# Kernel tuning notes

Hardware: AMD Instinct MI355X
Metric: run time of the kernel (lower is better)

Reference implementation:

```python
import jax, jax.numpy as jnp
import numpy as np

N_NODES = 50000
N_EDGES = 800000
N_FEAT = 128
N_HID = 128
N_CLS = 40
BN_EPS = 1e-5


def setup_inputs() -> dict:
    key = jax.random.key(0)
    ks = jax.random.split(key, 8)
    return {
        "x": jax.random.normal(ks[0], (N_NODES, N_FEAT), dtype=jnp.float32),
        "edge_index": jax.random.randint(ks[1], (2, N_EDGES), 0, N_NODES, dtype=jnp.int64),
        "W1l": jax.random.normal(ks[2], (N_HID, N_FEAT), dtype=jnp.float32) / np.sqrt(N_FEAT),
        "b1": jnp.zeros((N_HID,), dtype=jnp.float32),
        "W1r": jax.random.normal(ks[3], (N_HID, N_FEAT), dtype=jnp.float32) / np.sqrt(N_FEAT),
        "gamma": jnp.ones((N_HID,), dtype=jnp.float32),
        "beta": jnp.zeros((N_HID,), dtype=jnp.float32),
        "run_mean": jax.random.normal(ks[4], (N_HID,), dtype=jnp.float32) * 0.1,
        "run_var": jax.random.uniform(ks[5], (N_HID,), dtype=jnp.float32) + 0.5,
        "W2l": jax.random.normal(ks[6], (N_CLS, N_HID), dtype=jnp.float32) / np.sqrt(N_HID),
        "b2": jnp.zeros((N_CLS,), dtype=jnp.float32),
        "W2r": jax.random.normal(ks[7], (N_CLS, N_HID), dtype=jnp.float32) / np.sqrt(N_HID),
    }


def _sage_conv(h, src, dst, n_nodes, inv_deg, Wl, bl, Wr):
    # mean-aggregate neighbor features at each destination node
    agg = jax.ops.segment_sum(h[src], dst, num_segments=n_nodes)  # [N, D]
    agg = agg * inv_deg[:, None]
    # PyG SAGEConv: lin_l(aggr) (with bias) + lin_r(x) (no bias)
    return agg @ Wl.T + bl + h @ Wr.T


def reference(x, edge_index, W1l, b1, W1r, gamma, beta, run_mean, run_var, W2l, b2, W2r):
    src, dst = edge_index[0], edge_index[1]
    n = x.shape[0]
    deg = jax.ops.segment_sum(jnp.ones_like(src, dtype=x.dtype), dst, num_segments=n)
    inv_deg = 1.0 / jnp.maximum(deg, 1.0)
    h = _sage_conv(x, src, dst, n, inv_deg, W1l, b1, W1r)
    # transition: ReLU -> BatchNorm1d (eval: running stats) -> Dropout (identity in eval)
    h = jnp.maximum(h, 0.0)
    h = (h - run_mean) * (gamma / jnp.sqrt(run_var + BN_EPS)) + beta
    out = _sage_conv(h, src, dst, n, inv_deg, W2l, b2, W2r)
    return out
```

## Files before the change

### kernel.cpp

```cpp
#include <hip/hip_runtime.h>

#define N_NODES 50000
#define N_EDGES 800000
#define N_FEAT 128
#define N_HID 128
#define N_CLS 40
#define BN_EPS 1e-5f

#define CSR_STRIDE 64
#define NXCD 8
#define P_NODES 6250
#define CSR_B 1024
#define CSR_BO 128
#define WPACK_B 84
#define XPACK_B 3125

typedef short bf16x8 __attribute__((ext_vector_type(8)));
typedef float f32x4 __attribute__((ext_vector_type(4)));

__device__ __forceinline__ unsigned bfpack(float a, float b) {
    unsigned ua = __float_as_uint(a), ub = __float_as_uint(b);
    ua = (ua + 0x7FFFu + ((ua >> 16) & 1u)) >> 16;
    ub = (ub + 0x7FFFu + ((ub >> 16) & 1u)) >> 16;
    return ua | (ub << 16);
}
__device__ __forceinline__ unsigned short bfr1(float a) {
    unsigned u = __float_as_uint(a);
    u = (u + 0x7FFFu + ((u >> 16) & 1u)) >> 16;
    return (unsigned short)u;
}
__device__ __forceinline__ float bflo(unsigned u) { return __uint_as_float(u << 16); }
__device__ __forceinline__ float bfhi(unsigned u) { return __uint_as_float(u & 0xFFFF0000u); }

__global__ __launch_bounds__(256) void degprep_kernel(
    const int* __restrict__ src, const int* __restrict__ dst,
    int* __restrict__ deg_i, unsigned short* __restrict__ csr_pad,
    const float* __restrict__ W1l, const float* __restrict__ W1r,
    const float* __restrict__ W2l, const float* __restrict__ W2r,
    const float* __restrict__ x, unsigned* __restrict__ WfA,
    unsigned* __restrict__ WfB, unsigned* __restrict__ x_bf16) {
    int b = blockIdx.x;
    int t = threadIdx.x;
    if (b < CSR_B) {
        const int p = b & (NXCD - 1);
        const int bo = b >> 3;
        const int plo = p * P_NODES;
        const int phi = plo + P_NODES;
        const int4* dst4 = (const int4*)dst;
        const int4* src4 = (const int4*)src;
        for (int base = bo * 1024; base < N_EDGES; base += CSR_BO * 1024) {
            int e = base + t * 4;
            if (e < N_EDGES) {
                int4 d4 = dst4[(e >> 2)];
                int4 s4 = src4[(e >> 2)];
                if (d4.x >= plo && d4.x < phi) {
                    int r = atomicAdd(&deg_i[d4.x], 1);
                    if (r < CSR_STRIDE) csr_pad[d4.x * CSR_STRIDE + r] = (unsigned short)s4.x;
                }
                if (d4.y >= plo && d4.y < phi) {
                    int r = atomicAdd(&deg_i[d4.y], 1);
                    if (r < CSR_STRIDE) csr_pad[d4.y * CSR_STRIDE + r] = (unsigned short)s4.y;
                }
                if (d4.z >= plo && d4.z < phi) {
                    int r = atomicAdd(&deg_i[d4.z], 1);
                    if (r < CSR_STRIDE) csr_pad[d4.z * CSR_STRIDE + r] = (unsigned short)s4.z;
                }
                if (d4.w >= plo && d4.w < phi) {
                    int r = atomicAdd(&deg_i[d4.w], 1);
                    if (r < CSR_STRIDE) csr_pad[d4.w * CSR_STRIDE + r] = (unsigned short)s4.w;
                }
            }
        }
        return;
    }
    int i = (b - CSR_B) * 256 + t;
    if (b < CSR_B + WPACK_B) {
        if (i < 16384) {
            int f = i >> 8, r = i & 255;
            int lane = r >> 2, u = r & 3;
            int phase = f >> 5, kc = (f >> 3) & 3, nt = f & 7;
            int k0 = phase * 128 + kc * 32 + (lane >> 4) * 8 + u * 2;
            int n = nt * 16 + (lane & 15);
            float w0, w1;
            if (k0 < 128) {
                w0 = W1l[n * 128 + k0];
                w1 = W1l[n * 128 + k0 + 1];
            } else {
                w0 = W1r[n * 128 + k0 - 128];
                w1 = W1r[n * 128 + k0 - 127];
            }
            WfA[i] = bfpack(w0, w1);
        } else if (i < 21504) {
            int j = i - 16384;
            int f = j >> 8, r = j & 255;
            int lane = r >> 2, u = r & 3;
            int kc = f / 5, nt = f % 5;
            int k0 = kc * 32 + (lane >> 4) * 8 + u * 2;
            int n = nt * 16 + (lane & 15);
            float w0, w1;
            if (n < 40) {
                w0 = W2l[n * 128 + k0];
                w1 = W2l[n * 128 + k0 + 1];
            } else {
                w0 = W2r[(n - 40) * 128 + k0];
                w1 = W2r[(n - 40) * 128 + k0 + 1];
            }
            WfB[j] = bfpack(w0, w1);
        }
    } else {
        int j = (b - CSR_B - WPACK_B) * 256 + t;
        if (j < 800000) {
            const float4* xf = (const float4*)x;
            float4 a = xf[(size_t)j * 2];
            float4 bq = xf[(size_t)j * 2 + 1];
            uint4 o;
            o.x = bfpack(a.x, a.y);
            o.y = bfpack(a.z, a.w);
            o.z = bfpack(bq.x, bq.y);
            o.w = bfpack(bq.z, bq.w);
            ((uint4*)x_bf16)[j] = o;
        }
    }
}

__global__ __launch_bounds__(256) void gather1_kernel(const unsigned short* __restrict__ csr_pad,
                                                      const int* __restrict__ deg_i,
                                                      const unsigned* __restrict__ x_bf16,
                                                      unsigned* __restrict__ agg1b) {
    int sg = threadIdx.x >> 4;
    int li = threadIdx.x & 15;
    int gid = blockIdx.x * 16 + sg;
    if (gid >= N_NODES) return;
    int n = min(deg_i[gid], CSR_STRIDE);
    int beg = gid * CSR_STRIDE;
    int end = beg + n;
    const uint4* xb = (const uint4*)x_bf16;
    float acc[8];
#pragma unroll
    for (int j = 0; j < 8; ++j) acc[j] = 0.f;

    int e = beg;
    for (; e + 7 < end; e += 8) {
        uint4 tv[8];
#pragma unroll
        for (int q = 0; q < 8; ++q) {
            int s = csr_pad[e + q];
            tv[q] = xb[(size_t)s * 16 + li];
        }
#pragma unroll
        for (int q = 0; q < 8; ++q) {
            acc[0] += bflo(tv[q].x); acc[1] += bfhi(tv[q].x);
            acc[2] += bflo(tv[q].y); acc[3] += bfhi(tv[q].y);
            acc[4] += bflo(tv[q].z); acc[5] += bfhi(tv[q].z);
            acc[6] += bflo(tv[q].w); acc[7] += bfhi(tv[q].w);
        }
    }
    if (e + 3 < end) {
        uint4 tv[4];
#pragma unroll
        for (int q = 0; q < 4; ++q) {
            int s = csr_pad[e + q];
            tv[q] = xb[(size_t)s * 16 + li];
        }
#pragma unroll
        for (int q = 0; q < 4; ++q) {
            acc[0] += bflo(tv[q].x); acc[1] += bfhi(tv[q].x);
            acc[2] += bflo(tv[q].y); acc[3] += bfhi(tv[q].y);
            acc[4] += bflo(tv[q].z); acc[5] += bfhi(tv[q].z);
            acc[6] += bflo(tv[q].w); acc[7] += bfhi(tv[q].w);
        }
        e += 4;
    }
    for (; e < end; ++e) {
        int s = csr_pad[e];
        uint4 t0 = xb[(size_t)s * 16 + li];
        acc[0] += bflo(t0.x); acc[1] += bfhi(t0.x);
        acc[2] += bflo(t0.y); acc[3] += bfhi(t0.y);
        acc[4] += bflo(t0.z); acc[5] += bfhi(t0.z);
        acc[6] += bflo(t0.w); acc[7] += bfhi(t0.w);
    }
    float inv = 1.0f / fmaxf((float)n, 1.0f);
    uint4 o;
    o.x = bfpack(acc[0] * inv, acc[1] * inv);
    o.y = bfpack(acc[2] * inv, acc[3] * inv);
    o.z = bfpack(acc[4] * inv, acc[5] * inv);
    o.w = bfpack(acc[6] * inv, acc[7] * inv);
    ((uint4*)agg1b)[(size_t)gid * 16 + li] = o;
}

__global__ __launch_bounds__(256) void gemm_fused_kernel(
    const unsigned* __restrict__ agg1b, const unsigned* __restrict__ xb,
    const unsigned* __restrict__ WfA, const unsigned* __restrict__ WfB,
    const float* __restrict__ b1,
    const float* __restrict__ gamma, const float* __restrict__ beta,
    const float* __restrict__ rmean, const float* __restrict__ rvar,
    unsigned short* __restrict__ z2s, float* __restrict__ p2) {
    __shared__ unsigned Asu[64 * 68];
    const int t = threadIdx.x;
    const int wid = __builtin_amdgcn_readfirstlane(t >> 6);
    const int lane = t & 63;
    const int li = lane & 15;
    const int quad = lane >> 4;
    const int mbase = blockIdx.x * 64;

    f32x4 dacc[8];
#pragma unroll
    for (int nt = 0; nt < 8; ++nt) dacc[nt] = (f32x4){0.f, 0.f, 0.f, 0.f};

    for (int phase = 0; phase < 2; ++phase) {
        const unsigned* __restrict__ A = phase ? xb : agg1b;
        __syncthreads();
#pragma unroll
        for (int i = 0; i < 4; ++i) {
            int e = i * 256 + t;
            int row = e >> 4, seg = e & 15;
            int rr = mbase + row;
            rr = (rr < N_NODES) ? rr : N_NODES - 1;
            uint4 v = ((const uint4*)A)[(size_t)rr * 16 + seg];
            *(uint4*)&Asu[row * 68 + seg * 4] = v;
        }
        __syncthreads();
        bf16x8 af[4];
#pragma unroll
        for (int kc = 0; kc < 4; ++kc)
            af[kc] = *(const bf16x8*)&Asu[(wid * 16 + li) * 68 + kc * 16 + quad * 4];

        const unsigned* __restrict__ Wp = WfA + phase * 8192;
#pragma unroll
        for (int nt = 0; nt < 8; ++nt) {
#pragma unroll
            for (int kc = 0; kc < 4; ++kc) {
                bf16x8 bfr = *(const bf16x8*)(Wp + (size_t)(kc * 8 + nt) * 256 + lane * 4);
                dacc[nt] = __builtin_amdgcn_mfma_f32_16x16x32_bf16(af[kc], bfr, dacc[nt], 0, 0, 0);
            }
        }
    }

    __syncthreads();
    unsigned short* Hs = (unsigned short*)Asu;
#pragma unroll
    for (int nt = 0; nt < 8; ++nt) {
        int cg = nt * 16 + li;
        float sc = gamma[cg] * rsqrtf(rvar[cg] + BN_EPS);
        float sh = fmaf(-rmean[cg], sc, beta[cg]);
        float bb = b1[cg];
#pragma unroll
        for (int r = 0; r < 4; ++r) {
            int row = wid * 16 + quad * 4 + r;
            float pre = dacc[nt][r] + bb;
            Hs[row * 136 + cg] = bfr1(fmaf(fmaxf(pre, 0.f), sc, sh));
        }
    }
    __syncthreads();

    bf16x8 af2[4];
#pragma unroll
    for (int kc = 0; kc < 4; ++kc)
        af2[kc] = *(const bf16x8*)&Asu[(wid * 16 + li) * 68 + kc * 16 + quad * 4];

    f32x4 d2[5];
#pragma unroll
    for (int nt = 0; nt < 5; ++nt) d2[nt] = (f32x4){0.f, 0.f, 0.f, 0.f};
#pragma unroll
    for (int nt = 0; nt < 5; ++nt) {
#pragma unroll
        for (int kc = 0; kc < 4; ++kc) {
            bf16x8 bfr = *(const bf16x8*)(WfB + (size_t)(kc * 5 + nt) * 256 + lane * 4);
            d2[nt] = __builtin_amdgcn_mfma_f32_16x16x32_bf16(af2[kc], bfr, d2[nt], 0, 0, 0);
        }
    }

#pragma unroll
    for (int nt = 0; nt < 5; ++nt) {
        int cg = nt * 16 + li;
#pragma unroll
        for (int r = 0; r < 4; ++r) {
            int row = mbase + wid * 16 + quad * 4 + r;
            if (row < N_NODES) {
                float vv = d2[nt][r];
                if (cg < 40) z2s[(size_t)row * 40 + cg] = bfr1(vv);
                else p2[(size_t)row * 40 + (cg - 40)] = vv;
            }
        }
    }
}

__global__ __launch_bounds__(256) void gather2_kernel(const unsigned short* __restrict__ csr_pad,
                                                      const int* __restrict__ deg_i,
                                                      const unsigned short* __restrict__ z2s,
                                                      const float* __restrict__ p2,
                                                      const float* __restrict__ b2,
                                                      float* __restrict__ out) {
    int t = threadIdx.x;
    int sub = t / 10;
    int li = t - sub * 10;
    if (sub >= 25) return;
    int gid = blockIdx.x * 25 + sub;
    if (gid >= N_NODES) return;
    int n = min(deg_i[gid], CSR_STRIDE);
    int beg = gid * CSR_STRIDE;
    int end = beg + n;
    const uint2* z2 = (const uint2*)z2s;
    float4 acc = {0.f, 0.f, 0.f, 0.f};
    int e = beg;
    for (; e + 7 < end; e += 8) {
        uint2 tv[8];
#pragma unroll
        for (int q = 0; q < 8; ++q) {
            int s = csr_pad[e + q];
            tv[q] = z2[(size_t)s * 10 + li];
        }
#pragma unroll
        for (int q = 0; q < 8; ++q) {
            acc.x += bflo(tv[q].x); acc.y += bfhi(tv[q].x);
            acc.z += bflo(tv[q].y); acc.w += bfhi(tv[q].y);
        }
    }
    if (e + 3 < end) {
        uint2 tv[4];
#pragma unroll
        for (int q = 0; q < 4; ++q) {
            int s = csr_pad[e + q];
            tv[q] = z2[(size_t)s * 10 + li];
        }
#pragma unroll
        for (int q = 0; q < 4; ++q) {
            acc.x += bflo(tv[q].x); acc.y += bfhi(tv[q].x);
            acc.z += bflo(tv[q].y); acc.w += bfhi(tv[q].y);
        }
        e += 4;
    }
    for (; e < end; ++e) {
        int s = csr_pad[e];
        uint2 t0 = z2[(size_t)s * 10 + li];
        acc.x += bflo(t0.x); acc.y += bfhi(t0.x);
        acc.z += bflo(t0.y); acc.w += bfhi(t0.y);
    }
    float inv = 1.0f / fmaxf((float)n, 1.0f);
    float4 p = ((const float4*)p2)[(size_t)gid * 10 + li];
    float4 bb = ((const float4*)b2)[li];
    float4 r;
    r.x = fmaf(acc.x, inv, p.x + bb.x);
    r.y = fmaf(acc.y, inv, p.y + bb.y);
    r.z = fmaf(acc.z, inv, p.z + bb.z);
    r.w = fmaf(acc.w, inv, p.w + bb.w);
    ((float4*)out)[(size_t)gid * 10 + li] = r;
}

extern "C" void kernel_launch(void* const* d_in, const int* in_sizes, int n_in,
                              void* d_out, int out_size, void* d_ws, size_t ws_size,
                              hipStream_t stream) {
    const float* x     = (const float*)d_in[0];
    const int*   ei    = (const int*)d_in[1];
    const float* W1l   = (const float*)d_in[2];
    const float* b1    = (const float*)d_in[3];
    const float* W1r   = (const float*)d_in[4];
    const float* gamma = (const float*)d_in[5];
    const float* beta  = (const float*)d_in[6];
    const float* rmean = (const float*)d_in[7];
    const float* rvar  = (const float*)d_in[8];
    const float* W2l   = (const float*)d_in[9];
    const float* b2    = (const float*)d_in[10];
    const float* W2r   = (const float*)d_in[11];
    float* out = (float*)d_out;

    int* deg_i              = (int*)d_ws;
    unsigned short* csr_pad = (unsigned short*)(deg_i + 50048);
    unsigned* WfA           = (unsigned*)(deg_i + 50048 + 1600000);
    unsigned* WfB           = WfA + 16384;
    unsigned* x_bf16        = WfB + 5120;
    unsigned* agg1b         = x_bf16 + 3200000;
    unsigned short* z2s     = (unsigned short*)(agg1b + (size_t)50048 * 64);
    float* p2               = (float*)(z2s + (size_t)50048 * 40);

    const int* src = ei;
    const int* dst = ei + N_EDGES;

    hipMemsetAsync(deg_i, 0, (size_t)50048 * sizeof(int), stream);

    degprep_kernel<<<CSR_B + WPACK_B + XPACK_B, 256, 0, stream>>>(
        src, dst, deg_i, csr_pad, W1l, W1r, W2l, W2r, x, WfA, WfB, x_bf16);

    gather1_kernel<<<(N_NODES + 15) / 16, 256, 0, stream>>>(csr_pad, deg_i, x_bf16, agg1b);

    gemm_fused_kernel<<<(N_NODES + 63) / 64, 256, 0, stream>>>(
        agg1b, x_bf16, WfA, WfB, b1, gamma, beta, rmean, rvar, z2s, p2);

    gather2_kernel<<<(N_NODES + 24) / 25, 256, 0, stream>>>(csr_pad, deg_i, z2s, p2, b2, out);
}
```

Baseline: 195.7 us.

## Use hardware XCC id and per-partition atomic work queue for CSR build

The CSR-building blocks now read the physical XCC id from a hardware register to choose their destination-node partition, instead of inferring it from blockIdx. They pull 2048-edge chunks from a per-partition atomic counter instead of using a fixed stride. The aim is to keep each partition's deg/csr atomics local to one XCD's L2 and to balance load dynamically across blocks. This adds a global atomic plus two barriers per chunk. Correctness now depends on blocks being spread over all 8 XCCs: a partition whose XCC gets no CSR block would never be filled.

```diff
diff --git a/kernel.cpp b/kernel.cpp
--- a/kernel.cpp
+++ b/kernel.cpp
@@ -11,7 +11,8 @@
 #define NXCD 8
 #define P_NODES 6250
 #define CSR_B 1024
-#define CSR_BO 128
+#define CHUNK_E 2048
+#define N_CHUNK ((N_EDGES + CHUNK_E - 1) / CHUNK_E)
 #define WPACK_B 84
 #define XPACK_B 3125
 
@@ -34,7 +35,8 @@
 
 __global__ __launch_bounds__(256) void degprep_kernel(
     const int* __restrict__ src, const int* __restrict__ dst,
-    int* __restrict__ deg_i, unsigned short* __restrict__ csr_pad,
+    int* __restrict__ deg_i, int* __restrict__ wq,
+    unsigned short* __restrict__ csr_pad,
     const float* __restrict__ W1l, const float* __restrict__ W1r,
     const float* __restrict__ W2l, const float* __restrict__ W2r,
     const float* __restrict__ x, unsigned* __restrict__ WfA,
@@ -42,32 +44,41 @@
     int b = blockIdx.x;
     int t = threadIdx.x;
     if (b < CSR_B) {
-        const int p = b & (NXCD - 1);
-        const int bo = b >> 3;
+        unsigned xcc = __builtin_amdgcn_s_getreg(63508);
+        const int p = (int)(xcc & (NXCD - 1));
         const int plo = p * P_NODES;
         const int phi = plo + P_NODES;
         const int4* dst4 = (const int4*)dst;
         const int4* src4 = (const int4*)src;
-        for (int base = bo * 1024; base < N_EDGES; base += CSR_BO * 1024) {
-            int e = base + t * 4;
-            if (e < N_EDGES) {
-                int4 d4 = dst4[(e >> 2)];
-                int4 s4 = src4[(e >> 2)];
-                if (d4.x >= plo && d4.x < phi) {
-                    int r = atomicAdd(&deg_i[d4.x], 1);
-                    if (r < CSR_STRIDE) csr_pad[d4.x * CSR_STRIDE + r] = (unsigned short)s4.x;
-                }
-                if (d4.y >= plo && d4.y < phi) {
-                    int r = atomicAdd(&deg_i[d4.y], 1);
-                    if (r < CSR_STRIDE) csr_pad[d4.y * CSR_STRIDE + r] = (unsigned short)s4.y;
-                }
-                if (d4.z >= plo && d4.z < phi) {
-                    int r = atomicAdd(&deg_i[d4.z], 1);
-                    if (r < CSR_STRIDE) csr_pad[d4.z * CSR_STRIDE + r] = (unsigned short)s4.z;
-                }
-                if (d4.w >= plo && d4.w < phi) {
-                    int r = atomicAdd(&deg_i[d4.w], 1);
-                    if (r < CSR_STRIDE) csr_pad[d4.w * CSR_STRIDE + r] = (unsigned short)s4.w;
+        __shared__ int s_chunk;
+        for (;;) {
+            if (t == 0) s_chunk = atomicAdd(&wq[p], 1);
+            __syncthreads();
+            int base = s_chunk * CHUNK_E;
+            __syncthreads();
+            if (base >= N_EDGES) break;
+#pragma unroll
+            for (int off = 0; off < CHUNK_E; off += 1024) {
+                int e = base + off + t * 4;
+                if (e < N_EDGES) {
+                    int4 d4 = dst4[e >> 2];
+                    int4 s4 = src4[e >> 2];
+                    if (d4.x >= plo && d4.x < phi) {
+                        int r = atomicAdd(&deg_i[d4.x], 1);
+                        if (r < CSR_STRIDE) csr_pad[d4.x * CSR_STRIDE + r] = (unsigned short)s4.x;
+                    }
+                    if (d4.y >= plo && d4.y < phi) {
+                        int r = atomicAdd(&deg_i[d4.y], 1);
+                        if (r < CSR_STRIDE) csr_pad[d4.y * CSR_STRIDE + r] = (unsigned short)s4.y;
+                    }
+                    if (d4.z >= plo && d4.z < phi) {
+                        int r = atomicAdd(&deg_i[d4.z], 1);
+                        if (r < CSR_STRIDE) csr_pad[d4.z * CSR_STRIDE + r] = (unsigned short)s4.z;
+                    }
+                    if (d4.w >= plo && d4.w < phi) {
+                        int r = atomicAdd(&deg_i[d4.w], 1);
+                        if (r < CSR_STRIDE) csr_pad[d4.w * CSR_STRIDE + r] = (unsigned short)s4.w;
+                    }
                 }
             }
         }
@@ -365,8 +376,9 @@
     float* out = (float*)d_out;
 
     int* deg_i              = (int*)d_ws;
-    unsigned short* csr_pad = (unsigned short*)(deg_i + 50048);
-    unsigned* WfA           = (unsigned*)(deg_i + 50048 + 1600000);
+    int* wq                 = deg_i + 50048;
+    unsigned short* csr_pad = (unsigned short*)(wq + 16);
+    unsigned* WfA           = (unsigned*)(wq + 16 + 1600000);
     unsigned* WfB           = WfA + 16384;
     unsigned* x_bf16        = WfB + 5120;
     unsigned* agg1b         = x_bf16 + 3200000;
@@ -376,10 +388,10 @@
     const int* src = ei;
     const int* dst = ei + N_EDGES;
 
-    hipMemsetAsync(deg_i, 0, (size_t)50048 * sizeof(int), stream);
+    hipMemsetAsync(deg_i, 0, (size_t)(50048 + 16) * sizeof(int), stream);
 
     degprep_kernel<<<CSR_B + WPACK_B + XPACK_B, 256, 0, stream>>>(
-        src, dst, deg_i, csr_pad, W1l, W1r, W2l, W2r, x, WfA, WfB, x_bf16);
+        src, dst, deg_i, wq, csr_pad, W1l, W1r, W2l, W2r, x, WfA, WfB, x_bf16);
 
     gather1_kernel<<<(N_NODES + 15) / 16, 256, 0, stream>>>(csr_pad, deg_i, x_bf16, agg1b);
 
```

After: 230.3 us. +17.7%, slower.
